# Optimization experiments

Measured on AMD Instinct MI355X. Metric: run time of the kernel, lower is better.

## Reference

```python
import jax, jax.numpy as jnp
import numpy as np

N = 100000
E = 1600000
DIMS = [256, 128, 128, 64]
NEG_SLOPE_ATT = 0.2   # PyG GATConv attention leaky_relu
NEG_SLOPE_OUT = 0.01  # F.leaky_relu default between layers


def _glorot(key, shape):
    fan = sum(shape) if len(shape) > 1 else shape[0] + 1
    return jax.random.normal(key, shape, jnp.float32) * jnp.sqrt(2.0 / fan)


def make_params(key):
    params = {}
    for i in range(3):
        cin, cout = DIMS[i], DIMS[i + 1]
        ks = jax.random.split(jax.random.fold_in(key, i), 6)
        params[f"W{i+1}"] = _glorot(ks[0], (cin, cout))
        params[f"as{i+1}"] = _glorot(ks[1], (cout,))
        params[f"ad{i+1}"] = _glorot(ks[2], (cout,))
        params[f"We{i+1}"] = _glorot(ks[3], (1, cout))
        params[f"ae{i+1}"] = _glorot(ks[4], (cout,))
        params[f"b{i+1}"] = jnp.zeros((cout,), jnp.float32)
    return params


def setup_inputs() -> dict:
    key = jax.random.key(0)
    k1, k2, k3, kp = jax.random.split(key, 4)
    x = jax.random.normal(k1, (N, DIMS[0]), jnp.float32)
    edge_index = jax.random.randint(k2, (2, E), 0, N, jnp.int64)
    edge_weight = jax.random.uniform(k3, (E, 1), jnp.float32)
    inp = {"x": x, "edge_index": edge_index, "edge_weight": edge_weight}
    inp.update(make_params(kp))
    return inp


def _add_self_loops(src, dst, ew, n):
    # PyG fill_value='mean': per-target-node mean of edge_attr for loop attr
    deg = jax.ops.segment_sum(jnp.ones((src.shape[0],), jnp.float32), dst, num_segments=n)
    loop_attr = jax.ops.segment_sum(ew, dst, num_segments=n) / jnp.maximum(deg, 1.0)[:, None]
    loop = jnp.arange(n, dtype=src.dtype)
    return (jnp.concatenate([src, loop]), jnp.concatenate([dst, loop]),
            jnp.concatenate([ew, loop_attr], axis=0))


def gat_conv(x, src, dst, eattr, W, a_s, a_d, We, a_e, b):
    n = x.shape[0]
    h = x @ W                                # [N, C]
    alpha_src = (h @ a_s)[src]               # [Ef]
    alpha_dst = (h @ a_d)[dst]
    alpha_e = (eattr @ We) @ a_e             # [Ef]
    logits = jax.nn.leaky_relu(alpha_src + alpha_dst + alpha_e, NEG_SLOPE_ATT)
    m = jax.ops.segment_max(logits, dst, num_segments=n)
    ex = jnp.exp(logits - m[dst])
    denom = jax.ops.segment_sum(ex, dst, num_segments=n)
    alpha = ex / (denom[dst] + 1e-16)
    out = jax.ops.segment_sum(h[src] * alpha[:, None], dst, num_segments=n)
    return out + b


def reference(x, edge_index, edge_weight,
              W1, as1, ad1, We1, ae1, b1,
              W2, as2, ad2, We2, ae2, b2,
              W3, as3, ad3, We3, ae3, b3):
    n = x.shape[0]
    src, dst, ew = _add_self_loops(edge_index[0], edge_index[1], edge_weight, n)
    # dropout is identity in eval mode
    h = gat_conv(x, src, dst, ew, W1, as1, ad1, We1, ae1, b1)
    h = jax.nn.leaky_relu(h, NEG_SLOPE_OUT)
    h = gat_conv(h, src, dst, ew, W2, as2, ad2, We2, ae2, b2)
    h = jax.nn.leaky_relu(h, NEG_SLOPE_OUT)
    h = gat_conv(h, src, dst, ew, W3, as3, ad3, We3, ae3, b3)
    h = jax.nn.leaky_relu(h, NEG_SLOPE_OUT)
    return h
```

## Files before the change

### kernel.cpp

```cpp
#include <hip/hip_runtime.h>
#include <hip/hip_bf16.h>
#include <math.h>

#define NNODES 100000
#define NEDGES 1600000
#define MAXE 128
#define NSLICE 8
#define SL_SPAN ((NNODES + NSLICE - 1) / NSLICE)

typedef short bfrag8 __attribute__((ext_vector_type(8)));
typedef float facc4 __attribute__((ext_vector_type(4)));
typedef unsigned long long ull;

__device__ __forceinline__ unsigned short f2bf(float f) {
    unsigned u = __float_as_uint(f);
    unsigned r = u + 0x7fffu + ((u >> 16) & 1u);
    return (unsigned short)(r >> 16);
}
__device__ __forceinline__ float bf2f(unsigned short u) {
    return __uint_as_float((unsigned)u << 16);
}

__global__ void zero_i32(int* p, int n) {
    int i = blockIdx.x * blockDim.x + threadIdx.x;
    if (i < n) p[i] = 0;
}

__global__ void count_k(const int* __restrict__ ei, const float* __restrict__ ew,
                        ull* __restrict__ packed, unsigned short* __restrict__ rank16,
                        int E, int n) {
    int e = blockIdx.x * blockDim.x + threadIdx.x;
    if (e >= E) return;
    unsigned dstv = (unsigned)ei[E + e];
    unsigned short rk = 0;
    if (dstv < (unsigned)n) {
        unsigned fx = __float2uint_rn(ew[e] * 16777216.0f);
        ull old = atomicAdd(&packed[dstv], (1ULL << 40) | (ull)fx);
        unsigned r = (unsigned)(old >> 40);
        rk = (unsigned short)(r > 65535u ? 65535u : r);
    }
    rank16[e] = rk;
}

__global__ void scanA(const ull* __restrict__ packed, int* __restrict__ row_start,
                      int* __restrict__ blkSums, int n) {
    __shared__ int sdata[256];
    int tid = threadIdx.x;
    int base = blockIdx.x * 1024 + tid * 4;
    int v[4];
    int sum = 0;
#pragma unroll
    for (int j = 0; j < 4; j++) {
        int idx = base + j;
        int c = (idx < n) ? ((int)(packed[idx] >> 40) + 1) : 0;
        sum += c;
        v[j] = sum;
    }
    sdata[tid] = sum;
    __syncthreads();
    for (int off = 1; off < 256; off <<= 1) {
        int t = (tid >= off) ? sdata[tid - off] : 0;
        __syncthreads();
        sdata[tid] += t;
        __syncthreads();
    }
    int excl = sdata[tid] - sum;
#pragma unroll
    for (int j = 0; j < 4; j++) {
        int idx = base + j;
        if (idx < n) row_start[idx + 1] = excl + v[j];
    }
    if (tid == 255) blkSums[blockIdx.x] = sdata[255];
}

__global__ void scanB(int* __restrict__ blkSums, int nblk) {
    __shared__ int sdata[128];
    int tid = threadIdx.x;
    int v = (tid < nblk) ? blkSums[tid] : 0;
    sdata[tid] = v;
    __syncthreads();
    for (int off = 1; off < 128; off <<= 1) {
        int t = (tid >= off) ? sdata[tid - off] : 0;
        __syncthreads();
        sdata[tid] += t;
        __syncthreads();
    }
    if (tid < nblk) blkSums[tid] = sdata[tid] - v;
}

__global__ void scanC(int* __restrict__ row_start, const int* __restrict__ blkSums, int n) {
    int idx = blockIdx.x * blockDim.x + threadIdx.x;
    if (idx < n) row_start[idx + 1] += blkSums[idx >> 10];
    if (idx == 0) row_start[0] = 0;
}

__global__ void selfloop_k(const ull* __restrict__ packed, const int* __restrict__ row_start,
                           int2* __restrict__ eswr, int n) {
    int i = blockIdx.x * blockDim.x + threadIdx.x;
    if (i >= n) return;
    ull p = packed[i];
    int dg = (int)(p >> 40);
    float sum = (float)(p & 0xFFFFFFFFFFULL) * (1.0f / 16777216.0f);
    float w = sum / (float)(dg > 1 ? dg : 1);
    eswr[row_start[i]] = make_int2(i, __float_as_int(w));
}

__global__ __launch_bounds__(256) void scatter_k(
    const int* __restrict__ ei, const float* __restrict__ ew,
    const unsigned short* __restrict__ rank16, const int* __restrict__ row_start,
    int2* __restrict__ eswr, int E, int n) {
    int slice = blockIdx.x & (NSLICE - 1);
    int r = blockIdx.x >> 3;
    int bps = gridDim.x >> 3;
    int lo = slice * SL_SPAN;
    int hi = lo + SL_SPAN;
    for (int base = r * 256; base < E; base += bps * 256) {
        int e = base + threadIdx.x;
        if (e >= E) continue;
        int dst = ei[E + e];
        if (dst >= lo && dst < hi && (unsigned)dst < (unsigned)n) {
            int src = ei[e];
            if ((unsigned)src < (unsigned)n) {
                int pos = row_start[dst] + 1 + (int)rank16[e];
                eswr[pos] = make_int2(src, __float_as_int(ew[e]));
            }
        }
    }
}

__global__ void ce_k(const float* We1, const float* ae1,
                     const float* We2, const float* ae2,
                     const float* We3, const float* ae3, float* ce) {
    const float* W;
    const float* a;
    int cout;
    if (blockIdx.x == 0) { W = We1; a = ae1; cout = 128; }
    else if (blockIdx.x == 1) { W = We2; a = ae2; cout = 128; }
    else { W = We3; a = ae3; cout = 64; }
    int lane = threadIdx.x;
    float v = 0.f;
    for (int c = lane; c < cout; c += 64) v += W[c] * a[c];
    for (int o = 32; o; o >>= 1) v += __shfl_xor(v, o);
    if (lane == 0) ce[blockIdx.x] = v;
}

__global__ void wt_k(const float* __restrict__ W1, const float* __restrict__ W2,
                     const float* __restrict__ W3, unsigned short* __restrict__ wt1,
                     unsigned short* __restrict__ wt2, unsigned short* __restrict__ wt3) {
    int i = blockIdx.x * 256 + threadIdx.x;
    if (i < 32768) {
        int k = i >> 7, nn = i & 127;
        wt1[nn * 256 + k] = f2bf(W1[i]);
        return;
    }
    i -= 32768;
    if (i < 16384) {
        int k = i >> 7, nn = i & 127;
        wt2[nn * 128 + k] = f2bf(W2[i]);
        return;
    }
    i -= 16384;
    if (i < 8192) {
        int k = i >> 6, nn = i & 63;
        wt3[nn * 128 + k] = f2bf(W3[i]);
    }
}

__global__ __launch_bounds__(256) void gemm_mfma(
    const float* __restrict__ X, const unsigned short* __restrict__ Wt,
    unsigned short* __restrict__ H, const float* __restrict__ as_,
    const float* __restrict__ ad_, float* __restrict__ s, float* __restrict__ d,
    int nrows, int cin, int cout) {
    __shared__ __align__(16) unsigned short lA[64 * 40];
    __shared__ __align__(16) unsigned short lB[64 * 40];
    int t = threadIdx.x;
    int wv = t >> 6, lane = t & 63;
    int lr = lane & 15, lg = lane >> 4;
    int row0 = blockIdx.x * 64, col0 = blockIdx.y * 64;
    int sr = t >> 2, sc = (t & 3) * 8;

    facc4 acc[4] = {};

    const float* xrow = X + (size_t)(row0 + sr) * cin;
    bool rowok = (row0 + sr) < nrows;
    const unsigned short* wrow = Wt + (size_t)(col0 + sr) * cin;

    for (int k0 = 0; k0 < cin; k0 += 32) {
        union { bfrag8 v; unsigned short u[8]; } pa;
        if (rowok) {
            float4 v0 = *(const float4*)&xrow[k0 + sc];
            float4 v1 = *(const float4*)&xrow[k0 + sc + 4];
            pa.u[0] = f2bf(v0.x); pa.u[1] = f2bf(v0.y);
            pa.u[2] = f2bf(v0.z); pa.u[3] = f2bf(v0.w);
            pa.u[4] = f2bf(v1.x); pa.u[5] = f2bf(v1.y);
            pa.u[6] = f2bf(v1.z); pa.u[7] = f2bf(v1.w);
        } else {
#pragma unroll
            for (int j = 0; j < 8; j++) pa.u[j] = 0;
        }
        *(bfrag8*)&lA[sr * 40 + sc] = pa.v;
        *(bfrag8*)&lB[sr * 40 + sc] = *(const bfrag8*)&wrow[k0 + sc];
        __syncthreads();
        bfrag8 a = *(const bfrag8*)&lA[(wv * 16 + lr) * 40 + lg * 8];
#pragma unroll
        for (int n0 = 0; n0 < 4; n0++) {
            bfrag8 b = *(const bfrag8*)&lB[(n0 * 16 + lr) * 40 + lg * 8];
            acc[n0] = __builtin_amdgcn_mfma_f32_16x16x32_bf16(a, b, acc[n0], 0, 0, 0);
        }
        __syncthreads();
    }
#pragma unroll
    for (int r = 0; r < 4; r++) {
        int row = row0 + wv * 16 + lg * 4 + r;
        if (row >= nrows) continue;
        float ps = 0.f, pd = 0.f;
#pragma unroll
        for (int n0 = 0; n0 < 4; n0++) {
            int col = col0 + n0 * 16 + lr;
            float v = acc[n0][r];
            H[(size_t)row * cout + col] = f2bf(v);
            ps += v * as_[col];
            pd += v * ad_[col];
        }
        for (int o = 8; o; o >>= 1) {
            ps += __shfl_xor(ps, o);
            pd += __shfl_xor(pd, o);
        }
        if (lr == 0) {
            atomicAdd(&s[row], ps);
            atomicAdd(&d[row], pd);
        }
    }
}

__global__ __launch_bounds__(256) void agg_k(
    const int2* __restrict__ eswr, const int* __restrict__ row_start,
    const unsigned short* __restrict__ h, const float* __restrict__ s,
    const float* __restrict__ d, const float* __restrict__ ce_ptr,
    const float* __restrict__ bias, float* __restrict__ out, int n, int cout) {
    __shared__ float ex_s[4][MAXE];
    __shared__ int src_s[4][MAXE];
    int wslot = threadIdx.x >> 6;
    int wid = (blockIdx.x * blockDim.x + threadIdx.x) >> 6;
    int lane = threadIdx.x & 63;
    if (wid >= n) return;
    int lo = row_start[wid], ne = row_start[wid + 1] - lo;
    float ce = *ce_ptr;
    float di = d[wid];

    if (ne <= MAXE) {
        float m = -1e30f;
        for (int e = lane; e < ne; e += 64) {
            int2 ev = eswr[lo + e];
            float lg = s[ev.x] + di + ce * __int_as_float(ev.y);
            lg = lg > 0.f ? lg : 0.2f * lg;
            src_s[wslot][e] = ev.x;
            ex_s[wslot][e] = lg;
            m = fmaxf(m, lg);
        }
        for (int o = 32; o; o >>= 1) m = fmaxf(m, __shfl_xor(m, o));
        float den = 0.f;
        for (int e = lane; e < ne; e += 64) {
            float exv = __expf(ex_s[wslot][e] - m);
            ex_s[wslot][e] = exv;
            den += exv;
        }
        for (int o = 32; o; o >>= 1) den += __shfl_xor(den, o);
        float inv = 1.0f / (den + 1e-16f);

        if (cout == 128) {
            int half = lane >> 5, l32 = lane & 31;
            const ushort4* h4 = (const ushort4*)h;
            float a0 = 0.f, a1 = 0.f, a2 = 0.f, a3 = 0.f;
#pragma unroll 4
            for (int e = half; e < ne; e += 2) {
                float exv = ex_s[wslot][e];
                int src = src_s[wslot][e];
                ushort4 hv = h4[(size_t)src * 32 + l32];
                a0 += exv * bf2f(hv.x); a1 += exv * bf2f(hv.y);
                a2 += exv * bf2f(hv.z); a3 += exv * bf2f(hv.w);
            }
            a0 += __shfl_xor(a0, 32); a1 += __shfl_xor(a1, 32);
            a2 += __shfl_xor(a2, 32); a3 += __shfl_xor(a3, 32);
            if (half == 0) {
                float4 bv = ((const float4*)bias)[l32];
                float4 o;
                o.x = a0 * inv + bv.x; o.x = o.x > 0.f ? o.x : 0.01f * o.x;
                o.y = a1 * inv + bv.y; o.y = o.y > 0.f ? o.y : 0.01f * o.y;
                o.z = a2 * inv + bv.z; o.z = o.z > 0.f ? o.z : 0.01f * o.z;
                o.w = a3 * inv + bv.w; o.w = o.w > 0.f ? o.w : 0.01f * o.w;
                ((float4*)out)[(size_t)wid * 32 + l32] = o;
            }
        } else {
            int q = lane >> 4, l16 = lane & 15;
            const ushort4* h4 = (const ushort4*)h;
            float a0 = 0.f, a1 = 0.f, a2 = 0.f, a3 = 0.f;
#pragma unroll 4
            for (int e = q; e < ne; e += 4) {
                float exv = ex_s[wslot][e];
                int src = src_s[wslot][e];
                ushort4 hv = h4[(size_t)src * 16 + l16];
                a0 += exv * bf2f(hv.x); a1 += exv * bf2f(hv.y);
                a2 += exv * bf2f(hv.z); a3 += exv * bf2f(hv.w);
            }
            a0 += __shfl_xor(a0, 16); a1 += __shfl_xor(a1, 16);
            a2 += __shfl_xor(a2, 16); a3 += __shfl_xor(a3, 16);
            a0 += __shfl_xor(a0, 32); a1 += __shfl_xor(a1, 32);
            a2 += __shfl_xor(a2, 32); a3 += __shfl_xor(a3, 32);
            if (q == 0) {
                float4 bv = ((const float4*)bias)[l16];
                float4 o;
                o.x = a0 * inv + bv.x; o.x = o.x > 0.f ? o.x : 0.01f * o.x;
                o.y = a1 * inv + bv.y; o.y = o.y > 0.f ? o.y : 0.01f * o.y;
                o.z = a2 * inv + bv.z; o.z = o.z > 0.f ? o.z : 0.01f * o.z;
                o.w = a3 * inv + bv.w; o.w = o.w > 0.f ? o.w : 0.01f * o.w;
                ((float4*)out)[(size_t)wid * 16 + l16] = o;
            }
        }
        return;
    }

    float m = -1e30f;
    for (int e = lane; e < ne; e += 64) {
        int2 ev = eswr[lo + e];
        float lg = s[ev.x] + di + ce * __int_as_float(ev.y);
        lg = lg > 0.f ? lg : 0.2f * lg;
        m = fmaxf(m, lg);
    }
    for (int o = 32; o; o >>= 1) m = fmaxf(m, __shfl_xor(m, o));
    float den = 0.f;
    int c0 = lane, c1 = lane + 64;
    float a0 = 0.f, a1 = 0.f;
    for (int e = 0; e < ne; e++) {
        int2 ev = eswr[lo + e];
        float lg = s[ev.x] + di + ce * __int_as_float(ev.y);
        lg = lg > 0.f ? lg : 0.2f * lg;
        float ex = __expf(lg - m);
        den += ex;
        const unsigned short* hr = &h[(size_t)ev.x * cout];
        a0 += ex * bf2f(hr[c0]);
        if (cout > 64) a1 += ex * bf2f(hr[c1]);
    }
    float inv = 1.0f / (den + 1e-16f);
    float o0 = a0 * inv + bias[c0];
    o0 = o0 > 0.f ? o0 : 0.01f * o0;
    out[(size_t)wid * cout + c0] = o0;
    if (cout > 64) {
        float o1 = a1 * inv + bias[c1];
        o1 = o1 > 0.f ? o1 : 0.01f * o1;
        out[(size_t)wid * cout + c1] = o1;
    }
}

extern "C" void kernel_launch(void* const* d_in, const int* in_sizes, int n_in,
                              void* d_out, int out_size, void* d_ws, size_t ws_size,
                              hipStream_t stream) {
    const int N = NNODES, E = NEDGES, EF = NEDGES + NNODES;

    const float* x = (const float*)d_in[0];
    const int* ei = (const int*)d_in[1];
    const float* ew = (const float*)d_in[2];
    const float* W1 = (const float*)d_in[3];
    const float* as1 = (const float*)d_in[4];
    const float* ad1 = (const float*)d_in[5];
    const float* We1 = (const float*)d_in[6];
    const float* ae1 = (const float*)d_in[7];
    const float* b1 = (const float*)d_in[8];
    const float* W2 = (const float*)d_in[9];
    const float* as2 = (const float*)d_in[10];
    const float* ad2 = (const float*)d_in[11];
    const float* We2 = (const float*)d_in[12];
    const float* ae2 = (const float*)d_in[13];
    const float* b2 = (const float*)d_in[14];
    const float* W3 = (const float*)d_in[15];
    const float* as3 = (const float*)d_in[16];
    const float* ad3 = (const float*)d_in[17];
    const float* We3 = (const float*)d_in[18];
    const float* ae3 = (const float*)d_in[19];
    const float* b3 = (const float*)d_in[20];
    float* out = (float*)d_out;

    char* wp = (char*)d_ws;
    auto alloc = [&](size_t bytes, size_t align) -> void* {
        size_t a = ((size_t)wp + align - 1) & ~(align - 1);
        wp = (char*)(a + bytes);
        return (void*)a;
    };
    float* act = (float*)alloc((size_t)N * 128 * 4, 16);
    unsigned short* h = (unsigned short*)alloc((size_t)N * 128 * 2, 16);
    float* sd = (float*)alloc((size_t)6 * N * 4, 8);
    ull* packed = (ull*)alloc((size_t)N * 8, 8);
    int* row_start = (int*)alloc((size_t)(N + 1) * 4, 4);
    int* blkSums = (int*)alloc(128 * 4, 4);
    int2* eswr = (int2*)alloc((size_t)EF * 8, 8);
    unsigned short* rank16 = (unsigned short*)alloc((size_t)E * 2, 4);
    float* ce = (float*)alloc(4 * 4, 4);
    unsigned short* wt1 = (unsigned short*)alloc(32768 * 2, 16);
    unsigned short* wt2 = (unsigned short*)alloc(16384 * 2, 16);
    unsigned short* wt3 = (unsigned short*)alloc(8192 * 2, 16);

    zero_i32<<<(8 * N + 255) / 256, 256, 0, stream>>>((int*)sd, 8 * N);
    count_k<<<(E + 255) / 256, 256, 0, stream>>>(ei, ew, packed, rank16, E, N);
    int nblkA = (N + 1023) / 1024;
    scanA<<<nblkA, 256, 0, stream>>>(packed, row_start, blkSums, N);
    scanB<<<1, 128, 0, stream>>>(blkSums, nblkA);
    scanC<<<(N + 255) / 256, 256, 0, stream>>>(row_start, blkSums, N);
    selfloop_k<<<(N + 255) / 256, 256, 0, stream>>>(packed, row_start, eswr, N);
    scatter_k<<<NSLICE * 128, 256, 0, stream>>>(ei, ew, rank16, row_start, eswr, E, N);
    ce_k<<<3, 64, 0, stream>>>(We1, ae1, We2, ae2, We3, ae3, ce);
    wt_k<<<(32768 + 16384 + 8192) / 256, 256, 0, stream>>>(W1, W2, W3, wt1, wt2, wt3);

    {
        int cin = 256, cout = 128;
        dim3 grid((N + 63) / 64, cout / 64);
        gemm_mfma<<<grid, 256, 0, stream>>>(x, wt1, h, as1, ad1, sd + 0 * N, sd + 1 * N,
                                            N, cin, cout);
        agg_k<<<(N + 3) / 4, 256, 0, stream>>>(eswr, row_start, h, sd + 0 * N,
                                               sd + 1 * N, ce + 0, b1, act, N, cout);
    }
    {
        int cin = 128, cout = 128;
        dim3 grid((N + 63) / 64, cout / 64);
        gemm_mfma<<<grid, 256, 0, stream>>>(act, wt2, h, as2, ad2, sd + 2 * N, sd + 3 * N,
                                            N, cin, cout);
        agg_k<<<(N + 3) / 4, 256, 0, stream>>>(eswr, row_start, h, sd + 2 * N,
                                               sd + 3 * N, ce + 1, b2, act, N, cout);
    }
    {
        int cin = 128, cout = 64;
        dim3 grid((N + 63) / 64, cout / 64);
        gemm_mfma<<<grid, 256, 0, stream>>>(act, wt3, h, as3, ad3, sd + 4 * N, sd + 5 * N,
                                            N, cin, cout);
        agg_k<<<(N + 3) / 4, 256, 0, stream>>>(eswr, row_start, h, sd + 4 * N,
                                               sd + 5 * N, ce + 2, b3, out, N, cout);
    }
}
```

Measured before the change: 450.4 us.

## Pack edge records in count pass, fuse self-loops into scan, vectorize scatter

The count kernel now writes a packed (src, weight) record per edge, so the scatter kernel reads one int2 instead of separate src and weight arrays. Self-loop insertion moves into scanC, which removes one launch. The scatter kernel reads destinations four at a time with int4 loads, splits each slice into two sub-ranges to keep writes more local, and launches twice as many blocks. In exchange it adds an extra E*8-byte buffer and write, and it drops the src bounds check and the handling of E not divisible by 4.

```diff
diff --git a/kernel.cpp b/kernel.cpp
--- a/kernel.cpp
+++ b/kernel.cpp
@@ -6,6 +6,7 @@
 #define NEDGES 1600000
 #define MAXE 128
 #define NSLICE 8
+#define NSUB 2
 #define SL_SPAN ((NNODES + NSLICE - 1) / NSLICE)
 
 typedef short bfrag8 __attribute__((ext_vector_type(8)));
@@ -28,18 +29,21 @@
 
 __global__ void count_k(const int* __restrict__ ei, const float* __restrict__ ew,
                         ull* __restrict__ packed, unsigned short* __restrict__ rank16,
-                        int E, int n) {
+                        int2* __restrict__ erec, int E, int n) {
     int e = blockIdx.x * blockDim.x + threadIdx.x;
     if (e >= E) return;
+    int src = ei[e];
     unsigned dstv = (unsigned)ei[E + e];
+    float w = ew[e];
     unsigned short rk = 0;
     if (dstv < (unsigned)n) {
-        unsigned fx = __float2uint_rn(ew[e] * 16777216.0f);
+        unsigned fx = __float2uint_rn(w * 16777216.0f);
         ull old = atomicAdd(&packed[dstv], (1ULL << 40) | (ull)fx);
         unsigned r = (unsigned)(old >> 40);
         rk = (unsigned short)(r > 65535u ? 65535u : r);
     }
     rank16[e] = rk;
+    erec[e] = make_int2(src, __float_as_int(w));
 }
 
 __global__ void scanA(const ull* __restrict__ packed, int* __restrict__ row_start,
@@ -88,41 +92,55 @@
     if (tid < nblk) blkSums[tid] = sdata[tid] - v;
 }
 
-__global__ void scanC(int* __restrict__ row_start, const int* __restrict__ blkSums, int n) {
+__global__ void scanC(int* __restrict__ row_start, const int* __restrict__ blkSums,
+                      const ull* __restrict__ packed, int2* __restrict__ eswr, int n) {
     int idx = blockIdx.x * blockDim.x + threadIdx.x;
-    if (idx < n) row_start[idx + 1] += blkSums[idx >> 10];
+    if (idx < n) {
+        int v = row_start[idx + 1] + blkSums[idx >> 10];
+        row_start[idx + 1] = v;
+        ull p = packed[idx];
+        int cnt = (int)(p >> 40) + 1;
+        int dg = cnt - 1;
+        float sum = (float)(p & 0xFFFFFFFFFFULL) * (1.0f / 16777216.0f);
+        float w = sum / (float)(dg > 1 ? dg : 1);
+        eswr[v - cnt] = make_int2(idx, __float_as_int(w));
+    }
     if (idx == 0) row_start[0] = 0;
 }
 
-__global__ void selfloop_k(const ull* __restrict__ packed, const int* __restrict__ row_start,
-                           int2* __restrict__ eswr, int n) {
-    int i = blockIdx.x * blockDim.x + threadIdx.x;
-    if (i >= n) return;
-    ull p = packed[i];
-    int dg = (int)(p >> 40);
-    float sum = (float)(p & 0xFFFFFFFFFFULL) * (1.0f / 16777216.0f);
-    float w = sum / (float)(dg > 1 ? dg : 1);
-    eswr[row_start[i]] = make_int2(i, __float_as_int(w));
-}
-
 __global__ __launch_bounds__(256) void scatter_k(
-    const int* __restrict__ ei, const float* __restrict__ ew,
+    const int* __restrict__ ei_dst, const int2* __restrict__ erec,
     const unsigned short* __restrict__ rank16, const int* __restrict__ row_start,
     int2* __restrict__ eswr, int E, int n) {
     int slice = blockIdx.x & (NSLICE - 1);
     int r = blockIdx.x >> 3;
     int bps = gridDim.x >> 3;
-    int lo = slice * SL_SPAN;
-    int hi = lo + SL_SPAN;
-    for (int base = r * 256; base < E; base += bps * 256) {
-        int e = base + threadIdx.x;
-        if (e >= E) continue;
-        int dst = ei[E + e];
-        if (dst >= lo && dst < hi && (unsigned)dst < (unsigned)n) {
-            int src = ei[e];
-            if ((unsigned)src < (unsigned)n) {
-                int pos = row_start[dst] + 1 + (int)rank16[e];
-                eswr[pos] = make_int2(src, __float_as_int(ew[e]));
+    const int4* d4 = (const int4*)ei_dst;
+    int nq = E >> 2;
+    int span2 = (SL_SPAN + NSUB - 1) / NSUB;
+#pragma unroll
+    for (int sub = 0; sub < NSUB; sub++) {
+        int lo = slice * SL_SPAN + sub * span2;
+        int hi = lo + span2;
+        if (hi > n) hi = n;
+        for (int q = r * 256 + threadIdx.x; q < nq; q += bps * 256) {
+            int4 dv = d4[q];
+            int e = q * 4;
+            if (dv.x >= lo && dv.x < hi) {
+                int pos = row_start[dv.x] + 1 + (int)rank16[e];
+                eswr[pos] = erec[e];
+            }
+            if (dv.y >= lo && dv.y < hi) {
+                int pos = row_start[dv.y] + 1 + (int)rank16[e + 1];
+                eswr[pos] = erec[e + 1];
+            }
+            if (dv.z >= lo && dv.z < hi) {
+                int pos = row_start[dv.z] + 1 + (int)rank16[e + 2];
+                eswr[pos] = erec[e + 2];
+            }
+            if (dv.w >= lo && dv.w < hi) {
+                int pos = row_start[dv.w] + 1 + (int)rank16[e + 3];
+                eswr[pos] = erec[e + 3];
             }
         }
     }
@@ -393,6 +411,7 @@
     int* row_start = (int*)alloc((size_t)(N + 1) * 4, 4);
     int* blkSums = (int*)alloc(128 * 4, 4);
     int2* eswr = (int2*)alloc((size_t)EF * 8, 8);
+    int2* erec = (int2*)alloc((size_t)E * 8, 16);
     unsigned short* rank16 = (unsigned short*)alloc((size_t)E * 2, 4);
     float* ce = (float*)alloc(4 * 4, 4);
     unsigned short* wt1 = (unsigned short*)alloc(32768 * 2, 16);
@@ -400,13 +419,12 @@
     unsigned short* wt3 = (unsigned short*)alloc(8192 * 2, 16);
 
     zero_i32<<<(8 * N + 255) / 256, 256, 0, stream>>>((int*)sd, 8 * N);
-    count_k<<<(E + 255) / 256, 256, 0, stream>>>(ei, ew, packed, rank16, E, N);
+    count_k<<<(E + 255) / 256, 256, 0, stream>>>(ei, ew, packed, rank16, erec, E, N);
     int nblkA = (N + 1023) / 1024;
     scanA<<<nblkA, 256, 0, stream>>>(packed, row_start, blkSums, N);
     scanB<<<1, 128, 0, stream>>>(blkSums, nblkA);
-    scanC<<<(N + 255) / 256, 256, 0, stream>>>(row_start, blkSums, N);
-    selfloop_k<<<(N + 255) / 256, 256, 0, stream>>>(packed, row_start, eswr, N);
-    scatter_k<<<NSLICE * 128, 256, 0, stream>>>(ei, ew, rank16, row_start, eswr, E, N);
+    scanC<<<(N + 255) / 256, 256, 0, stream>>>(row_start, blkSums, packed, eswr, N);
+    scatter_k<<<NSLICE * 256, 256, 0, stream>>>(ei + E, erec, rank16, row_start, eswr, E, N);
     ce_k<<<3, 64, 0, stream>>>(We1, ae1, We2, ae2, We3, ae3, ce);
     wt_k<<<(32768 + 16384 + 8192) / 256, 256, 0, stream>>>(W1, W2, W3, wt1, wt2, wt3);
 
```

Result: no change. 445.5 us (-1.1%).

## Build CSR via two-pass bucket sort and store intermediate activations in bf16

Applied to the files above, without the earlier changes.

The old CSR build did global atomics per edge, a three-kernel scan, a self-loop pass and a multi-pass sliced scatter. It is replaced by a block-local bucket sort into 256-node buckets with fixed-capacity regions, a single small scan, and a per-bucket placement kernel that computes degrees, self-loop weights and row starts in shared memory. Setup kernels are merged into one init launch, and inter-layer activations are written in bf16 so the next GEMM reads half the bytes. Any bucket holding more than CAP edges silently drops the excess. The edge order within a row now becomes nondeterministic.

```diff
diff --git a/kernel.cpp b/kernel.cpp
--- a/kernel.cpp
+++ b/kernel.cpp
@@ -5,8 +5,11 @@
 #define NNODES 100000
 #define NEDGES 1600000
 #define MAXE 128
-#define NSLICE 8
-#define SL_SPAN ((NNODES + NSLICE - 1) / NSLICE)
+#define NB 391
+#define CAP 6144
+#define EPT 7
+#define BK_EDGES (256 * EPT)
+#define BK_BLOCKS ((NEDGES + BK_EDGES - 1) / BK_EDGES)
 
 typedef short bfrag8 __attribute__((ext_vector_type(8)));
 typedef float facc4 __attribute__((ext_vector_type(4)));
@@ -21,153 +24,194 @@
     return __uint_as_float((unsigned)u << 16);
 }
 
-__global__ void zero_i32(int* p, int n) {
-    int i = blockIdx.x * blockDim.x + threadIdx.x;
-    if (i < n) p[i] = 0;
-}
-
-__global__ void count_k(const int* __restrict__ ei, const float* __restrict__ ew,
-                        ull* __restrict__ packed, unsigned short* __restrict__ rank16,
-                        int E, int n) {
-    int e = blockIdx.x * blockDim.x + threadIdx.x;
-    if (e >= E) return;
-    unsigned dstv = (unsigned)ei[E + e];
-    unsigned short rk = 0;
-    if (dstv < (unsigned)n) {
-        unsigned fx = __float2uint_rn(ew[e] * 16777216.0f);
-        ull old = atomicAdd(&packed[dstv], (1ULL << 40) | (ull)fx);
-        unsigned r = (unsigned)(old >> 40);
-        rk = (unsigned short)(r > 65535u ? 65535u : r);
-    }
-    rank16[e] = rk;
-}
-
-__global__ void scanA(const ull* __restrict__ packed, int* __restrict__ row_start,
-                      int* __restrict__ blkSums, int n) {
-    __shared__ int sdata[256];
-    int tid = threadIdx.x;
-    int base = blockIdx.x * 1024 + tid * 4;
-    int v[4];
-    int sum = 0;
-#pragma unroll
-    for (int j = 0; j < 4; j++) {
-        int idx = base + j;
-        int c = (idx < n) ? ((int)(packed[idx] >> 40) + 1) : 0;
-        sum += c;
-        v[j] = sum;
-    }
-    sdata[tid] = sum;
-    __syncthreads();
-    for (int off = 1; off < 256; off <<= 1) {
-        int t = (tid >= off) ? sdata[tid - off] : 0;
-        __syncthreads();
-        sdata[tid] += t;
-        __syncthreads();
-    }
-    int excl = sdata[tid] - sum;
-#pragma unroll
-    for (int j = 0; j < 4; j++) {
-        int idx = base + j;
-        if (idx < n) row_start[idx + 1] = excl + v[j];
-    }
-    if (tid == 255) blkSums[blockIdx.x] = sdata[255];
-}
-
-__global__ void scanB(int* __restrict__ blkSums, int nblk) {
-    __shared__ int sdata[128];
-    int tid = threadIdx.x;
-    int v = (tid < nblk) ? blkSums[tid] : 0;
-    sdata[tid] = v;
-    __syncthreads();
-    for (int off = 1; off < 128; off <<= 1) {
-        int t = (tid >= off) ? sdata[tid - off] : 0;
-        __syncthreads();
-        sdata[tid] += t;
-        __syncthreads();
-    }
-    if (tid < nblk) blkSums[tid] = sdata[tid] - v;
-}
-
-__global__ void scanC(int* __restrict__ row_start, const int* __restrict__ blkSums, int n) {
-    int idx = blockIdx.x * blockDim.x + threadIdx.x;
-    if (idx < n) row_start[idx + 1] += blkSums[idx >> 10];
-    if (idx == 0) row_start[0] = 0;
-}
-
-__global__ void selfloop_k(const ull* __restrict__ packed, const int* __restrict__ row_start,
-                           int2* __restrict__ eswr, int n) {
-    int i = blockIdx.x * blockDim.x + threadIdx.x;
-    if (i >= n) return;
-    ull p = packed[i];
-    int dg = (int)(p >> 40);
-    float sum = (float)(p & 0xFFFFFFFFFFULL) * (1.0f / 16777216.0f);
-    float w = sum / (float)(dg > 1 ? dg : 1);
-    eswr[row_start[i]] = make_int2(i, __float_as_int(w));
-}
-
-__global__ __launch_bounds__(256) void scatter_k(
-    const int* __restrict__ ei, const float* __restrict__ ew,
-    const unsigned short* __restrict__ rank16, const int* __restrict__ row_start,
-    int2* __restrict__ eswr, int E, int n) {
-    int slice = blockIdx.x & (NSLICE - 1);
-    int r = blockIdx.x >> 3;
-    int bps = gridDim.x >> 3;
-    int lo = slice * SL_SPAN;
-    int hi = lo + SL_SPAN;
-    for (int base = r * 256; base < E; base += bps * 256) {
-        int e = base + threadIdx.x;
-        if (e >= E) continue;
-        int dst = ei[E + e];
-        if (dst >= lo && dst < hi && (unsigned)dst < (unsigned)n) {
-            int src = ei[e];
-            if ((unsigned)src < (unsigned)n) {
-                int pos = row_start[dst] + 1 + (int)rank16[e];
-                eswr[pos] = make_int2(src, __float_as_int(ew[e]));
-            }
-        }
-    }
-}
-
-__global__ void ce_k(const float* We1, const float* ae1,
-                     const float* We2, const float* ae2,
-                     const float* We3, const float* ae3, float* ce) {
-    const float* W;
-    const float* a;
-    int cout;
-    if (blockIdx.x == 0) { W = We1; a = ae1; cout = 128; }
-    else if (blockIdx.x == 1) { W = We2; a = ae2; cout = 128; }
-    else { W = We3; a = ae3; cout = 64; }
-    int lane = threadIdx.x;
-    float v = 0.f;
-    for (int c = lane; c < cout; c += 64) v += W[c] * a[c];
-    for (int o = 32; o; o >>= 1) v += __shfl_xor(v, o);
-    if (lane == 0) ce[blockIdx.x] = v;
-}
-
-__global__ void wt_k(const float* __restrict__ W1, const float* __restrict__ W2,
-                     const float* __restrict__ W3, unsigned short* __restrict__ wt1,
-                     unsigned short* __restrict__ wt2, unsigned short* __restrict__ wt3) {
-    int i = blockIdx.x * 256 + threadIdx.x;
-    if (i < 32768) {
-        int k = i >> 7, nn = i & 127;
-        wt1[nn * 256 + k] = f2bf(W1[i]);
+__global__ void init_k(int* zbase,
+                       const float* __restrict__ W1, const float* __restrict__ W2,
+                       const float* __restrict__ W3, unsigned short* __restrict__ wt1,
+                       unsigned short* __restrict__ wt2, unsigned short* __restrict__ wt3,
+                       const float* We1, const float* ae1, const float* We2,
+                       const float* ae2, const float* We3, const float* ae3, float* ce) {
+    int gb = blockIdx.x, t = threadIdx.x;
+    if (gb < 2369) {
+        int i = gb * 256 + t;
+        if (i < 6 * NNODES + NB * 16) zbase[i] = 0;
         return;
     }
-    i -= 32768;
-    if (i < 16384) {
-        int k = i >> 7, nn = i & 127;
-        wt2[nn * 128 + k] = f2bf(W2[i]);
-        return;
-    }
-    i -= 16384;
-    if (i < 8192) {
+    if (gb < 2593) {
+        int i = (gb - 2369) * 256 + t;
+        if (i < 32768) {
+            int k = i >> 7, nn = i & 127;
+            wt1[nn * 256 + k] = f2bf(W1[i]);
+            return;
+        }
+        i -= 32768;
+        if (i < 16384) {
+            int k = i >> 7, nn = i & 127;
+            wt2[nn * 128 + k] = f2bf(W2[i]);
+            return;
+        }
+        i -= 16384;
         int k = i >> 6, nn = i & 63;
         wt3[nn * 128 + k] = f2bf(W3[i]);
-    }
-}
-
+        return;
+    }
+    if (t >= 64) return;
+    int cb = gb - 2593;
+    const float* W; const float* a; int cout;
+    if (cb == 0) { W = We1; a = ae1; cout = 128; }
+    else if (cb == 1) { W = We2; a = ae2; cout = 128; }
+    else { W = We3; a = ae3; cout = 64; }
+    float v = 0.f;
+    for (int c = t; c < cout; c += 64) v += W[c] * a[c];
+    for (int o = 32; o; o >>= 1) v += __shfl_xor(v, o);
+    if (t == 0) ce[cb] = v;
+}
+
+__global__ __launch_bounds__(256) void bucket_k(
+    const int* __restrict__ ei, const float* __restrict__ ew,
+    unsigned* __restrict__ fill , uint2* __restrict__ regions) {
+    __shared__ unsigned cnt[NB], lbase[NB], gb_s[NB], cur[NB];
+    __shared__ unsigned ssum[256];
+    __shared__ uint2 srec[BK_EDGES];
+    __shared__ unsigned short sbkt[BK_EDGES];
+    int t = threadIdx.x;
+    for (int b = t; b < NB; b += 256) cnt[b] = 0;
+    __syncthreads();
+    int e0 = blockIdx.x * BK_EDGES;
+    int dstv[EPT], srcv[EPT];
+    unsigned wb[EPT];
+#pragma unroll
+    for (int j = 0; j < EPT; j++) {
+        int e = e0 + j * 256 + t;
+        dstv[j] = -1;
+        if (e < NEDGES) {
+            int dd = ei[NEDGES + e];
+            int ss = ei[e];
+            if ((unsigned)dd < (unsigned)NNODES && (unsigned)ss < (unsigned)NNODES) {
+                dstv[j] = dd; srcv[j] = ss; wb[j] = __float_as_uint(ew[e]);
+            }
+        }
+        if (dstv[j] >= 0) atomicAdd(&cnt[dstv[j] >> 8], 1u);
+    }
+    __syncthreads();
+    unsigned c0 = cnt[t];
+    unsigned c1 = (t + 256 < NB) ? cnt[t + 256] : 0u;
+    ssum[t] = c0 + c1;
+    __syncthreads();
+    for (int off = 1; off < 256; off <<= 1) {
+        unsigned v = (t >= off) ? ssum[t - off] : 0u;
+        __syncthreads();
+        ssum[t] += v;
+        __syncthreads();
+    }
+    unsigned excl = ssum[t] - (c0 + c1);
+    lbase[t] = excl; cur[t] = excl;
+    gb_s[t] = c0 ? atomicAdd(&fill[t * 16], c0) : 0u;
+    if (t + 256 < NB) {
+        lbase[t + 256] = excl + c0; cur[t + 256] = excl + c0;
+        gb_s[t + 256] = c1 ? atomicAdd(&fill[(t + 256) * 16], c1) : 0u;
+    }
+    __syncthreads();
+#pragma unroll
+    for (int j = 0; j < EPT; j++) {
+        if (dstv[j] >= 0) {
+            unsigned b = (unsigned)dstv[j] >> 8;
+            unsigned p = atomicAdd(&cur[b], 1u);
+            srec[p] = make_uint2(((unsigned)(dstv[j] & 255) << 24) | (unsigned)srcv[j], wb[j]);
+            sbkt[p] = (unsigned short)b;
+        }
+    }
+    __syncthreads();
+    unsigned tot = ssum[255];
+    for (unsigned i = t; i < tot; i += 256) {
+        unsigned b = sbkt[i];
+        unsigned slot = gb_s[b] + (i - lbase[b]);
+        if (slot < CAP) regions[(size_t)b * CAP + slot] = srec[i];
+    }
+}
+
+__global__ void bucket_scan_k(const unsigned* __restrict__ fill,
+                              unsigned* __restrict__ bucket_base, int* __restrict__ row_start) {
+    __shared__ unsigned s[512];
+    int t = threadIdx.x;
+    unsigned c = 0;
+    if (t < NB) {
+        unsigned sz = fill[t * 16];
+        if (sz > CAP) sz = CAP;
+        int nv = NNODES - (t << 8);
+        if (nv > 256) nv = 256;
+        if (nv < 0) nv = 0;
+        c = sz + (unsigned)nv;
+    }
+    s[t] = c;
+    __syncthreads();
+    for (int off = 1; off < 512; off <<= 1) {
+        unsigned v = (t >= off) ? s[t - off] : 0u;
+        __syncthreads();
+        s[t] += v;
+        __syncthreads();
+    }
+    if (t < NB) bucket_base[t] = s[t] - c;
+    if (t == 511) row_start[NNODES] = (int)s[511];
+}
+
+__global__ __launch_bounds__(512) void place_k(
+    const uint2* __restrict__ regions, const unsigned* __restrict__ fill,
+    const unsigned* __restrict__ bucket_base, int2* __restrict__ eswr,
+    int* __restrict__ row_start) {
+    __shared__ uint2 rec[CAP];
+    __shared__ unsigned deg[256], sumw[256], sc[256], seg[256], cur[256];
+    int b = blockIdx.x, t = threadIdx.x;
+    unsigned size = fill[b * 16];
+    if (size > CAP) size = CAP;
+    int dst0 = b << 8;
+    int nvalid = NNODES - dst0;
+    if (nvalid > 256) nvalid = 256;
+    if (nvalid < 0) nvalid = 0;
+    if (t < 256) { deg[t] = 0; sumw[t] = 0; }
+    __syncthreads();
+    for (unsigned i = t; i < size; i += 512) {
+        uint2 r = regions[(size_t)b * CAP + i];
+        rec[i] = r;
+        unsigned dl = r.x >> 24;
+        atomicAdd(&deg[dl], 1u);
+        atomicAdd(&sumw[dl], __float2uint_rn(__uint_as_float(r.y) * 16777216.0f));
+    }
+    __syncthreads();
+    unsigned cnti = (t < (unsigned)nvalid) ? deg[t] + 1u : 0u;
+    if (t < 256) sc[t] = cnti;
+    __syncthreads();
+    for (int off = 1; off < 256; off <<= 1) {
+        unsigned v = (t >= off && t < 256) ? sc[t - off] : 0u;
+        __syncthreads();
+        if (t < 256) sc[t] += v;
+        __syncthreads();
+    }
+    unsigned bb = bucket_base[b];
+    if (t < 256) {
+        unsigned excl = sc[t] - cnti;
+        seg[t] = excl;
+        cur[t] = excl + 1u;
+        if (t < (unsigned)nvalid) {
+            int dst = dst0 + t;
+            row_start[dst] = (int)(bb + excl);
+            float sw = (float)sumw[t] * (1.0f / 16777216.0f);
+            int dg = (int)deg[t];
+            float w = sw / (float)(dg > 1 ? dg : 1);
+            eswr[bb + excl] = make_int2(dst, __float_as_int(w));
+        }
+    }
+    __syncthreads();
+    for (unsigned i = t; i < size; i += 512) {
+        uint2 r = rec[i];
+        unsigned dl = r.x >> 24;
+        unsigned p = atomicAdd(&cur[dl], 1u);
+        eswr[bb + p] = make_int2((int)(r.x & 0xFFFFFFu), (int)r.y);
+    }
+}
+
+template <bool ABF16>
 __global__ __launch_bounds__(256) void gemm_mfma(
-    const float* __restrict__ X, const unsigned short* __restrict__ Wt,
+    const void* __restrict__ Xv, const unsigned short* __restrict__ Wt,
     unsigned short* __restrict__ H, const float* __restrict__ as_,
     const float* __restrict__ ad_, float* __restrict__ s, float* __restrict__ d,
     int nrows, int cin, int cout) {
@@ -180,20 +224,24 @@
     int sr = t >> 2, sc = (t & 3) * 8;
 
     facc4 acc[4] = {};
-
-    const float* xrow = X + (size_t)(row0 + sr) * cin;
     bool rowok = (row0 + sr) < nrows;
     const unsigned short* wrow = Wt + (size_t)(col0 + sr) * cin;
 
     for (int k0 = 0; k0 < cin; k0 += 32) {
         union { bfrag8 v; unsigned short u[8]; } pa;
         if (rowok) {
-            float4 v0 = *(const float4*)&xrow[k0 + sc];
-            float4 v1 = *(const float4*)&xrow[k0 + sc + 4];
-            pa.u[0] = f2bf(v0.x); pa.u[1] = f2bf(v0.y);
-            pa.u[2] = f2bf(v0.z); pa.u[3] = f2bf(v0.w);
-            pa.u[4] = f2bf(v1.x); pa.u[5] = f2bf(v1.y);
-            pa.u[6] = f2bf(v1.z); pa.u[7] = f2bf(v1.w);
+            if constexpr (ABF16) {
+                const unsigned short* xrow = (const unsigned short*)Xv + (size_t)(row0 + sr) * cin;
+                pa.v = *(const bfrag8*)&xrow[k0 + sc];
+            } else {
+                const float* xrow = (const float*)Xv + (size_t)(row0 + sr) * cin;
+                float4 v0 = *(const float4*)&xrow[k0 + sc];
+                float4 v1 = *(const float4*)&xrow[k0 + sc + 4];
+                pa.u[0] = f2bf(v0.x); pa.u[1] = f2bf(v0.y);
+                pa.u[2] = f2bf(v0.z); pa.u[3] = f2bf(v0.w);
+                pa.u[4] = f2bf(v1.x); pa.u[5] = f2bf(v1.y);
+                pa.u[6] = f2bf(v1.z); pa.u[7] = f2bf(v1.w);
+            }
         } else {
 #pragma unroll
             for (int j = 0; j < 8; j++) pa.u[j] = 0;
@@ -204,8 +252,8 @@
         bfrag8 a = *(const bfrag8*)&lA[(wv * 16 + lr) * 40 + lg * 8];
 #pragma unroll
         for (int n0 = 0; n0 < 4; n0++) {
-            bfrag8 b = *(const bfrag8*)&lB[(n0 * 16 + lr) * 40 + lg * 8];
-            acc[n0] = __builtin_amdgcn_mfma_f32_16x16x32_bf16(a, b, acc[n0], 0, 0, 0);
+            bfrag8 bfr = *(const bfrag8*)&lB[(n0 * 16 + lr) * 40 + lg * 8];
+            acc[n0] = __builtin_amdgcn_mfma_f32_16x16x32_bf16(a, bfr, acc[n0], 0, 0, 0);
         }
         __syncthreads();
     }
@@ -233,11 +281,12 @@
     }
 }
 
+template <bool OBF16>
 __global__ __launch_bounds__(256) void agg_k(
     const int2* __restrict__ eswr, const int* __restrict__ row_start,
     const unsigned short* __restrict__ h, const float* __restrict__ s,
     const float* __restrict__ d, const float* __restrict__ ce_ptr,
-    const float* __restrict__ bias, float* __restrict__ out, int n, int cout) {
+    const float* __restrict__ bias, void* __restrict__ outv, int n, int cout) {
     __shared__ float ex_s[4][MAXE];
     __shared__ int src_s[4][MAXE];
     int wslot = threadIdx.x >> 6;
@@ -289,7 +338,13 @@
                 o.y = a1 * inv + bv.y; o.y = o.y > 0.f ? o.y : 0.01f * o.y;
                 o.z = a2 * inv + bv.z; o.z = o.z > 0.f ? o.z : 0.01f * o.z;
                 o.w = a3 * inv + bv.w; o.w = o.w > 0.f ? o.w : 0.01f * o.w;
-                ((float4*)out)[(size_t)wid * 32 + l32] = o;
+                if constexpr (OBF16) {
+                    ushort4 ov;
+                    ov.x = f2bf(o.x); ov.y = f2bf(o.y); ov.z = f2bf(o.z); ov.w = f2bf(o.w);
+                    ((ushort4*)outv)[(size_t)wid * 32 + l32] = ov;
+                } else {
+                    ((float4*)outv)[(size_t)wid * 32 + l32] = o;
+                }
             }
         } else {
             int q = lane >> 4, l16 = lane & 15;
@@ -314,7 +369,13 @@
                 o.y = a1 * inv + bv.y; o.y = o.y > 0.f ? o.y : 0.01f * o.y;
                 o.z = a2 * inv + bv.z; o.z = o.z > 0.f ? o.z : 0.01f * o.z;
                 o.w = a3 * inv + bv.w; o.w = o.w > 0.f ? o.w : 0.01f * o.w;
-                ((float4*)out)[(size_t)wid * 16 + l16] = o;
+                if constexpr (OBF16) {
+                    ushort4 ov;
+                    ov.x = f2bf(o.x); ov.y = f2bf(o.y); ov.z = f2bf(o.z); ov.w = f2bf(o.w);
+                    ((ushort4*)outv)[(size_t)wid * 16 + l16] = ov;
+                } else {
+                    ((float4*)outv)[(size_t)wid * 16 + l16] = o;
+                }
             }
         }
         return;
@@ -344,11 +405,19 @@
     float inv = 1.0f / (den + 1e-16f);
     float o0 = a0 * inv + bias[c0];
     o0 = o0 > 0.f ? o0 : 0.01f * o0;
-    out[(size_t)wid * cout + c0] = o0;
+    float o1 = 0.f;
     if (cout > 64) {
-        float o1 = a1 * inv + bias[c1];
+        o1 = a1 * inv + bias[c1];
         o1 = o1 > 0.f ? o1 : 0.01f * o1;
-        out[(size_t)wid * cout + c1] = o1;
+    }
+    if constexpr (OBF16) {
+        unsigned short* out = (unsigned short*)outv;
+        out[(size_t)wid * cout + c0] = f2bf(o0);
+        if (cout > 64) out[(size_t)wid * cout + c1] = f2bf(o1);
+    } else {
+        float* out = (float*)outv;
+        out[(size_t)wid * cout + c0] = o0;
+        if (cout > 64) out[(size_t)wid * cout + c1] = o1;
     }
 }
 
@@ -386,52 +455,47 @@
         wp = (char*)(a + bytes);
         return (void*)a;
     };
-    float* act = (float*)alloc((size_t)N * 128 * 4, 16);
+    float* sd = (float*)alloc((size_t)6 * N * 4, 16);
+    unsigned* fill = (unsigned*)alloc((size_t)NB * 16 * 4, 4);
+    unsigned short* act = (unsigned short*)alloc((size_t)N * 128 * 2, 16);
     unsigned short* h = (unsigned short*)alloc((size_t)N * 128 * 2, 16);
-    float* sd = (float*)alloc((size_t)6 * N * 4, 8);
-    ull* packed = (ull*)alloc((size_t)N * 8, 8);
     int* row_start = (int*)alloc((size_t)(N + 1) * 4, 4);
-    int* blkSums = (int*)alloc(128 * 4, 4);
-    int2* eswr = (int2*)alloc((size_t)EF * 8, 8);
-    unsigned short* rank16 = (unsigned short*)alloc((size_t)E * 2, 4);
+    unsigned* bucket_base = (unsigned*)alloc((size_t)NB * 4, 4);
+    int2* eswr = (int2*)alloc((size_t)EF * 8, 16);
+    uint2* regions = (uint2*)alloc((size_t)NB * CAP * 8, 16);
     float* ce = (float*)alloc(4 * 4, 4);
     unsigned short* wt1 = (unsigned short*)alloc(32768 * 2, 16);
     unsigned short* wt2 = (unsigned short*)alloc(16384 * 2, 16);
     unsigned short* wt3 = (unsigned short*)alloc(8192 * 2, 16);
 
-    zero_i32<<<(8 * N + 255) / 256, 256, 0, stream>>>((int*)sd, 8 * N);
-    count_k<<<(E + 255) / 256, 256, 0, stream>>>(ei, ew, packed, rank16, E, N);
-    int nblkA = (N + 1023) / 1024;
-    scanA<<<nblkA, 256, 0, stream>>>(packed, row_start, blkSums, N);
-    scanB<<<1, 128, 0, stream>>>(blkSums, nblkA);
-    scanC<<<(N + 255) / 256, 256, 0, stream>>>(row_start, blkSums, N);
-    selfloop_k<<<(N + 255) / 256, 256, 0, stream>>>(packed, row_start, eswr, N);
-    scatter_k<<<NSLICE * 128, 256, 0, stream>>>(ei, ew, rank16, row_start, eswr, E, N);
-    ce_k<<<3, 64, 0, stream>>>(We1, ae1, We2, ae2, We3, ae3, ce);
-    wt_k<<<(32768 + 16384 + 8192) / 256, 256, 0, stream>>>(W1, W2, W3, wt1, wt2, wt3);
+    init_k<<<2596, 256, 0, stream>>>((int*)sd, W1, W2, W3, wt1, wt2, wt3,
+                                     We1, ae1, We2, ae2, We3, ae3, ce);
+    bucket_k<<<BK_BLOCKS, 256, 0, stream>>>(ei, ew, fill, regions);
+    bucket_scan_k<<<1, 512, 0, stream>>>(fill, bucket_base, row_start);
+    place_k<<<NB, 512, 0, stream>>>(regions, fill, bucket_base, eswr, row_start);
 
     {
         int cin = 256, cout = 128;
         dim3 grid((N + 63) / 64, cout / 64);
-        gemm_mfma<<<grid, 256, 0, stream>>>(x, wt1, h, as1, ad1, sd + 0 * N, sd + 1 * N,
-                                            N, cin, cout);
-        agg_k<<<(N + 3) / 4, 256, 0, stream>>>(eswr, row_start, h, sd + 0 * N,
-                                               sd + 1 * N, ce + 0, b1, act, N, cout);
+        gemm_mfma<false><<<grid, 256, 0, stream>>>(x, wt1, h, as1, ad1,
+                                                   sd + 0 * N, sd + 1 * N, N, cin, cout);
+        agg_k<true><<<(N + 3) / 4, 256, 0, stream>>>(eswr, row_start, h, sd + 0 * N,
+                                                     sd + 1 * N, ce + 0, b1, act, N, cout);
     }
     {
         int cin = 128, cout = 128;
         dim3 grid((N + 63) / 64, cout / 64);
-        gemm_mfma<<<grid, 256, 0, stream>>>(act, wt2, h, as2, ad2, sd + 2 * N, sd + 3 * N,
-                                            N, cin, cout);
-        agg_k<<<(N + 3) / 4, 256, 0, stream>>>(eswr, row_start, h, sd + 2 * N,
-                                               sd + 3 * N, ce + 1, b2, act, N, cout);
+        gemm_mfma<true><<<grid, 256, 0, stream>>>(act, wt2, h, as2, ad2,
+                                                  sd + 2 * N, sd + 3 * N, N, cin, cout);
+        agg_k<true><<<(N + 3) / 4, 256, 0, stream>>>(eswr, row_start, h, sd + 2 * N,
+                                                     sd + 3 * N, ce + 1, b2, act, N, cout);
     }
     {
         int cin = 128, cout = 64;
         dim3 grid((N + 63) / 64, cout / 64);
-        gemm_mfma<<<grid, 256, 0, stream>>>(act, wt3, h, as3, ad3, sd + 4 * N, sd + 5 * N,
-                                            N, cin, cout);
-        agg_k<<<(N + 3) / 4, 256, 0, stream>>>(eswr, row_start, h, sd + 4 * N,
-                                               sd + 5 * N, ce + 2, b3, out, N, cout);
-    }
-}
+        gemm_mfma<true><<<grid, 256, 0, stream>>>(act, wt3, h, as3, ad3,
+                                                  sd + 4 * N, sd + 5 * N, N, cin, cout);
+        agg_k<false><<<(N + 3) / 4, 256, 0, stream>>>(eswr, row_start, h, sd + 4 * N,
+                                                      sd + 5 * N, ce + 2, b3, out, N, cout);
+    }
+}
```

Measured after the change: 387.0 us. -14.1%, faster.
